# Performance work log

Measured on AMD Instinct MI355X. Metric: run time of the kernel, lower is better.

Reference implementation:

```python
import jax, jax.numpy as jnp
import numpy as np

B, S, HID = 2, 2048, 1024
H, D = 16, 64
KD = H * D
RMS_EPS = 1e-5
L2_EPS = 1e-12


def setup_inputs() -> dict:
    key = jax.random.key(0)
    ks = jax.random.split(key, 9)
    w = lambda k, shape: jax.random.normal(k, shape, jnp.float32) * 0.02
    return {
        "x": jax.random.normal(ks[0], (B, S, HID), jnp.float32),
        "Wq": w(ks[1], (HID, KD)),
        "Wk": w(ks[2], (HID, KD)),
        "Wv": w(ks[3], (HID, KD)),
        "Wf": w(ks[4], (HID, KD)),
        "Wb": w(ks[5], (HID, H)),
        "A_log": jnp.log(jnp.full((H,), 8.0, jnp.float32)),
        "dt_bias": jnp.zeros((KD,), jnp.float32),
        "Wg": w(ks[6], (HID, KD)),
        "bg": jnp.zeros((KD,), jnp.float32),
        "Wo": w(ks[7], (KD, HID)),
        "norm_w": jnp.ones((D,), jnp.float32),
    }


def _l2norm(t):
    n = jnp.sqrt(jnp.sum(t * t, axis=-1, keepdims=True))
    return t / jnp.clip(n, L2_EPS)


def reference(x, Wq, Wk, Wv, Wf, Wb, A_log, dt_bias, Wg, bg, Wo, norm_w):
    b, s, _ = x.shape
    h = A_log.shape[0]
    d = norm_w.shape[0]

    q = jax.nn.silu(x @ Wq).reshape(b, s, h, d)
    k = jax.nn.silu(x @ Wk).reshape(b, s, h, d)
    v = jax.nn.silu(x @ Wv).reshape(b, s, h, d)
    g = (x @ Wf).reshape(b, s, h, d)
    beta = jax.nn.sigmoid(x @ Wb)  # [b,s,h]

    q = _l2norm(q)
    k = _l2norm(k)
    g = jax.nn.sigmoid(g - dt_bias.reshape(h, d))
    A = jnp.exp(-jnp.exp(A_log))  # [h]

    # seq-major for scan: [s, b, h, d]
    qs = jnp.moveaxis(q, 1, 0)
    kss = jnp.moveaxis(k, 1, 0)
    vs = jnp.moveaxis(v, 1, 0)
    gs = jnp.moveaxis(g, 1, 0)
    bs = jnp.moveaxis(beta, 1, 0)  # [s,b,h]

    state0 = jnp.zeros((b, h, d, d), x.dtype)

    def step(state, inp):
        q_t, k_t, v_t, g_t, b_t = inp
        o_t = jnp.einsum('bhd,bhde->bhe', q_t, state) * g_t
        state = A[None, :, None, None] * state \
            + b_t[..., None, None] * (k_t[..., :, None] * v_t[..., None, :])
        return state, o_t

    _, o = jax.lax.scan(step, state0, (qs, kss, vs, gs, bs))
    o = jnp.moveaxis(o, 0, 1)  # [b,s,h,d]

    # RMSNorm over head_dim, then gate
    o = o * jax.lax.rsqrt(jnp.mean(o * o, axis=-1, keepdims=True) + RMS_EPS) * norm_w
    gate = jax.nn.sigmoid(x @ Wg + bg).reshape(b, s, h, d)
    o = (o * gate).reshape(b, s, h * d)
    return o @ Wo
```

## Files before the change

kernel.cpp:

```cpp
#include <hip/hip_runtime.h>
#include <hip/hip_bf16.h>

typedef __hip_bfloat16 bf16;
typedef __attribute__((ext_vector_type(8))) short v8s;
typedef __attribute__((ext_vector_type(4))) short v4s;
typedef __attribute__((ext_vector_type(4))) float v4f;

#define MFMA16(a,b,c) __builtin_amdgcn_mfma_f32_16x16x32_bf16((a),(b),(c),0,0,0)
#define SCHED0() __builtin_amdgcn_sched_barrier(0)


static const size_t OFF_XBF    = 0;
static const size_t OFF_WCATT  = 8388608;
static const size_t OFF_WOT    = OFF_WCATT + 11010048;
static const size_t OFF_Y      = OFF_WOT + 2097152;
static const size_t OFF_BETA   = OFF_Y + 41943040;
static const size_t OFF_OPRE   = OFF_XBF;

__device__ __forceinline__ void gl2lds16(const bf16* g, bf16* l) {
  __builtin_amdgcn_global_load_lds(
      (const __attribute__((address_space(1))) void*)g,
      (__attribute__((address_space(3))) void*)l, 16, 0, 0);
}

__global__ __launch_bounds__(256) void prep(
    const float* __restrict__ x,
    const float* __restrict__ W0, const float* __restrict__ W1,
    const float* __restrict__ W2, const float* __restrict__ W3,
    const float* __restrict__ W4, const float* __restrict__ W5,
    const float* __restrict__ Wb,
    bf16* __restrict__ xb, bf16* __restrict__ WcatT, bf16* __restrict__ WoT)
{
  __shared__ float tile[64][65];
  int bid = blockIdx.x;
  if (bid < 2048) {
    int t = bid * 256 + threadIdx.x;
    int row = t >> 7, ch = t & 127;
    const float* src = x + (size_t)row * 1024 + ch * 8;
    v4f v0 = *(const v4f*)src;
    v4f v1 = *(const v4f*)(src + 4);
    union { bf16 h[8]; v8s s; } u;
    for (int i = 0; i < 4; ++i) { u.h[i] = __float2bfloat16(v0[i]); u.h[4+i] = __float2bfloat16(v1[i]); }
    int ch2 = (ch & ~3) | ((ch ^ (row >> 1)) & 3);
    *(v8s*)(xb + (size_t)row * 1024 + ch2 * 8) = u.s;
  } else if (bid < 3584) {
    int b2 = bid - 2048;
    int mi = b2 >> 8;
    int rem = b2 & 255;
    int c0 = (rem & 15) * 64;
    int r0 = (rem >> 4) * 64;
    const float* W = (mi==0)?W0:(mi==1)?W1:(mi==2)?W2:(mi==3)?W3:(mi==4)?W4:W5;
    bf16* out = (mi < 5) ? (WcatT + (size_t)mi * 1048576) : WoT;
    int l = threadIdx.x & 63, w = threadIdx.x >> 6;
    for (int i = 0; i < 16; ++i)
      tile[w + 4*i][l] = W[(size_t)(r0 + w + 4*i) * 1024 + c0 + l];
    __syncthreads();
    for (int i = 0; i < 16; ++i) {
      int orow = c0 + w + 4*i;
      int q = l >> 3;
      int q2 = (mi < 5) ? ((q & ~3) | ((q ^ (orow >> 1)) & 3))
                        : ((q ^ orow) & 7);
      int col = r0 + (q2 << 3) + (l & 7);
      out[(size_t)orow * 1024 + col] = __float2bfloat16(tile[l][w + 4*i]);
    }
  } else {
    int j = (bid - 3584) * 2 + (threadIdx.x >> 7);
    int ch = threadIdx.x & 127;
    union { bf16 h[8]; v8s s; } u;
    for (int i = 0; i < 8; ++i)
      u.h[i] = __float2bfloat16(j < 16 ? Wb[(size_t)(ch*8 + i) * 16 + j] : 0.f);
    int row = 5120 + j;
    int ch2 = (ch & ~3) | ((ch ^ (row >> 1)) & 3);
    *(v8s*)(WcatT + (size_t)row * 1024 + ch2 * 8) = u.s;
  }
}

__global__ __launch_bounds__(256, 2) void gemm_main(
    const bf16* __restrict__ A, const bf16* __restrict__ BT,
    bf16* __restrict__ Yb, const float* __restrict__ dtb,
    const float* __restrict__ bgp, float* __restrict__ betaOut)
{
  __shared__ bf16 As[2][4096];
  __shared__ bf16 Bs[2][8192];
  const int tid = threadIdx.x;
  const int xcd = (int)blockIdx.x & 7, p = (int)blockIdx.x >> 3;
  const int by = xcd * 4 + (p & 3);
  const int bx = p >> 2;
  const int m0 = by * 128, n0 = bx * 256;
  const int w = tid >> 6, l = tid & 63;
  const int wr = w >> 1, wc = w & 1;
  const int lr = l & 15, lkq = l >> 4;
  const int cq = ((lkq ^ ((lr >> 1) & 3)) << 3);
  const int arow0 = (wr * 64 + lr) * 32;
  const int brow0 = (wc * 128 + lr) * 32;

  v4f acc[4][8];
  #pragma unroll
  for (int i = 0; i < 4; ++i)
    #pragma unroll
    for (int j = 0; j < 8; ++j) acc[i][j] = (v4f){0.f,0.f,0.f,0.f};

#define STG(t_, buf_) do { \
  gl2lds16(&A[(size_t)(m0 + (tid >> 2)) * 1024 + (t_)*32 + (tid & 3)*8], \
           &As[buf_][tid*8]); \
  gl2lds16(&A[(size_t)(m0 + 64 + (tid >> 2)) * 1024 + (t_)*32 + (tid & 3)*8], \
           &As[buf_][2048 + tid*8]); \
  gl2lds16(&BT[(size_t)(n0 + (tid >> 2)) * 1024 + (t_)*32 + (tid & 3)*8], \
           &Bs[buf_][tid*8]); \
  gl2lds16(&BT[(size_t)(n0 + 64 + (tid >> 2)) * 1024 + (t_)*32 + (tid & 3)*8], \
           &Bs[buf_][2048 + tid*8]); \
  gl2lds16(&BT[(size_t)(n0 + 128 + (tid >> 2)) * 1024 + (t_)*32 + (tid & 3)*8], \
           &Bs[buf_][4096 + tid*8]); \
  gl2lds16(&BT[(size_t)(n0 + 192 + (tid >> 2)) * 1024 + (t_)*32 + (tid & 3)*8], \
           &Bs[buf_][6144 + tid*8]); \
} while(0)

  STG(0, 0); SCHED0();
  STG(1, 1); SCHED0();

  for (int t = 0; t < 32; ++t) {
    const int cur = t & 1;
    if (t == 31) { asm volatile("s_waitcnt vmcnt(0)" ::: "memory"); }
    else         { asm volatile("s_waitcnt vmcnt(6)" ::: "memory"); }
    SCHED0();
    __builtin_amdgcn_s_barrier();
    SCHED0();
    const bf16* Ab = &As[cur][0];
    const bf16* Bb = &Bs[cur][0];
    v8s afr[4], bfr[8];
    #pragma unroll
    for (int mt = 0; mt < 4; ++mt)
      afr[mt] = *(const v8s*)(Ab + arow0 + mt*512 + cq);
    #pragma unroll
    for (int nt = 0; nt < 8; ++nt)
      bfr[nt] = *(const v8s*)(Bb + brow0 + nt*512 + cq);
    asm volatile("s_waitcnt lgkmcnt(0)" ::: "memory");
    SCHED0();
    __builtin_amdgcn_s_barrier();
    SCHED0();
    if (t + 2 < 32) { STG(t + 2, cur); }
    __builtin_amdgcn_s_setprio(1);
    #pragma unroll
    for (int mt = 0; mt < 4; ++mt)
      #pragma unroll
      for (int nt = 0; nt < 8; ++nt)
        acc[mt][nt] = MFMA16(afr[mt], bfr[nt], acc[mt][nt]);
    __builtin_amdgcn_s_setprio(0);
  }
#undef STG

  const int region = (n0 + wc * 128) >> 10;
  #pragma unroll
  for (int mt = 0; mt < 4; ++mt)
    #pragma unroll
    for (int r = 0; r < 4; ++r) {
      int gm = m0 + wr * 64 + mt * 16 + lkq * 4 + r;
      float v[8];
      if (region < 2) {
        #pragma unroll
        for (int hh = 0; hh < 2; ++hh) {
          float ss = 0.f;
          #pragma unroll
          for (int q4 = 0; q4 < 4; ++q4) {
            float y = acc[mt][hh*4 + q4][r];
            float s = y / (1.f + __expf(-y));
            v[hh*4 + q4] = s; ss += s * s;
          }
          ss += __shfl_xor(ss, 1, 64); ss += __shfl_xor(ss, 2, 64);
          ss += __shfl_xor(ss, 4, 64); ss += __shfl_xor(ss, 8, 64);
          float inv = 1.f / fmaxf(sqrtf(ss), 1e-12f);
          #pragma unroll
          for (int q4 = 0; q4 < 4; ++q4) v[hh*4 + q4] *= inv;
        }
      } else if (region == 2) {
        #pragma unroll
        for (int nt = 0; nt < 8; ++nt) {
          float y = acc[mt][nt][r];
          v[nt] = y / (1.f + __expf(-y));
        }
      } else if (region == 3) {
        #pragma unroll
        for (int nt = 0; nt < 8; ++nt) {
          int gn = n0 + wc * 128 + nt * 16 + lr;
          float z = acc[mt][nt][r] - dtb[gn & 1023];
          v[nt] = 1.f / (1.f + __expf(-z));
        }
      } else if (region == 4) {
        #pragma unroll
        for (int nt = 0; nt < 8; ++nt) {
          int gn = n0 + wc * 128 + nt * 16 + lr;
          float z = acc[mt][nt][r] + bgp[gn & 1023];
          v[nt] = 1.f / (1.f + __expf(-z));
        }
      } else {
        #pragma unroll
        for (int nt = 0; nt < 8; ++nt) {
          int gn = n0 + wc * 128 + nt * 16 + lr;
          if (gn < 5136)
            betaOut[(size_t)gm * 16 + (gn - 5120)] =
                1.f / (1.f + __expf(-acc[mt][nt][r]));
        }
        continue;
      }
      #pragma unroll
      for (int nt = 0; nt < 8; ++nt) {
        int gn = n0 + wc * 128 + nt * 16 + lr;
        Yb[(size_t)gm * 5120 + gn] = __float2bfloat16(v[nt]);
      }
    }
}

__global__ __launch_bounds__(256) void gemm_out(
    const bf16* __restrict__ A, const bf16* __restrict__ BT,
    float* __restrict__ Co)
{
  __shared__ bf16 As[2][8192];
  __shared__ bf16 Bs[2][8192];
  const int tid = threadIdx.x;
  int swzb = ((int)blockIdx.x & 7) * 32 + ((int)blockIdx.x >> 3);
  const int by = swzb >> 3, bx = swzb & 7;
  const int m0 = by * 128, n0 = bx * 128;
  const int w = tid >> 6, l = tid & 63;
  const int wm = (w >> 1) * 64, wn = (w & 1) * 64;
  const int lr = l & 15, lkq = l >> 4;
  const int xorv = lr & 7;
  const int c0 = ((lkq ^ xorv) << 3), c1 = (((4 + lkq) ^ xorv) << 3);
  v4f acc[4][4];
  for (int i = 0; i < 4; ++i) for (int j = 0; j < 4; ++j) acc[i][j] = (v4f){0.f,0.f,0.f,0.f};

#define STAGE(kk, buf) \
  for (int i_ = 0; i_ < 4; ++i_) { \
    int eo_ = (i_ * 256 + tid) * 8; \
    int r_ = eo_ >> 6, cc_ = eo_ & 63; \
    gl2lds16(&A[(size_t)(m0 + r_) * 1024 + (kk) + cc_], &As[buf][eo_]); \
    gl2lds16(&BT[(size_t)(n0 + r_) * 1024 + (kk) + cc_], &Bs[buf][eo_]); \
  }

  STAGE(0, 0);
  __syncthreads();
  int cur = 0;
  for (int kk = 0; kk < 1024; kk += 64) {
    if (kk + 64 < 1024) { STAGE(kk + 64, cur ^ 1); }
    v8s af[2][4], bfr[2][4];
    #pragma unroll
    for (int mt = 0; mt < 4; ++mt) {
      af[0][mt] = *(const v8s*)(&As[cur][(wm + mt*16 + lr) * 64 + c0]);
      af[1][mt] = *(const v8s*)(&As[cur][(wm + mt*16 + lr) * 64 + c1]);
      bfr[0][mt] = *(const v8s*)(&Bs[cur][(wn + mt*16 + lr) * 64 + c0]);
      bfr[1][mt] = *(const v8s*)(&Bs[cur][(wn + mt*16 + lr) * 64 + c1]);
    }
    #pragma unroll
    for (int kc = 0; kc < 2; ++kc)
      #pragma unroll
      for (int mt = 0; mt < 4; ++mt)
        #pragma unroll
        for (int nt = 0; nt < 4; ++nt)
          acc[mt][nt] = MFMA16(af[kc][mt], bfr[kc][nt], acc[mt][nt]);
    __syncthreads();
    cur ^= 1;
  }
#undef STAGE
  #pragma unroll
  for (int mt = 0; mt < 4; ++mt)
    #pragma unroll
    for (int nt = 0; nt < 4; ++nt)
      #pragma unroll
      for (int r = 0; r < 4; ++r) {
        int gm = m0 + wm + mt*16 + lkq*4 + r;
        int gn = n0 + wn + nt*16 + lr;
        Co[(size_t)gm * 1024 + gn] = acc[mt][nt][r];
      }
}

__global__ __launch_bounds__(256) void passFused(
    const bf16* __restrict__ Y, const float* __restrict__ beta,
    const float* __restrict__ A_log, const float* __restrict__ norm_w,
    bf16* __restrict__ opre)
{
  int c = blockIdx.x, bh = blockIdx.y;
  int b = bh >> 4, h = bh & 15;
  int row0 = b * 2048 + c * 64;
  int prow0 = row0 - 64;
  bool hasPrev = (c > 0);
  __shared__ bf16 Qs[64][72], Ks[64][72], Vt[64][72];
  __shared__ bf16 Kp[64][72], Vp[64][72];
  __shared__ bf16 Ps[64][72], St[64][72];
  __shared__ float betas[64], pw[64];
  int tid = threadIdx.x, w = tid >> 6, l = tid & 63;
  float aexp = __expf(A_log[h]);
  if (tid < 64) {
    pw[tid] = __expf(-aexp * (float)tid);
    betas[tid] = beta[(size_t)(row0 + tid) * 16 + h];
  }
  __syncthreads();
  for (int i = 0; i < 2; ++i) {
    int cid = i * 256 + tid;
    int r = cid >> 3, c8 = (cid & 7) * 8;
    size_t ybase = (size_t)(row0 + r) * 5120 + h * 64 + c8;
    v8s q8 = *(const v8s*)(&Y[ybase]);
    v8s k8 = *(const v8s*)(&Y[ybase + 1024]);
    v8s v8 = *(const v8s*)(&Y[ybase + 2048]);
    *(v8s*)(&Qs[r][c8]) = q8;
    *(v8s*)(&Ks[r][c8]) = k8;
    const bf16* vpt = (const bf16*)&v8;
    for (int jj = 0; jj < 8; ++jj) Vt[c8 + jj][r] = vpt[jj];
    if (hasPrev) {
      size_t pbase = (size_t)(prow0 + r) * 5120 + h * 64 + c8;
      v8s pk8 = *(const v8s*)(&Y[pbase + 1024]);
      v8s pv8 = *(const v8s*)(&Y[pbase + 2048]);
      float coefT = pw[63 - r] * beta[(size_t)(prow0 + r) * 16 + h];
      const bf16* pkp = (const bf16*)&pk8;
      const bf16* pvp = (const bf16*)&pv8;
      for (int jj = 0; jj < 8; ++jj) {
        Kp[c8 + jj][r] = __float2bfloat16(coefT * __bfloat162float(pkp[jj]));
        Vp[c8 + jj][r] = pvp[jj];
      }
    } else {
      bf16 z = __float2bfloat16(0.f);
      for (int jj = 0; jj < 8; ++jj) { Kp[c8 + jj][r] = z; Vp[c8 + jj][r] = z; }
    }
  }
  __syncthreads();
  const int lr = l & 15, lk = (l >> 4) * 8;
  v4f accT[4], accP[4];
  for (int nt = 0; nt < 4; ++nt) { accT[nt] = (v4f){0.f,0.f,0.f,0.f}; accP[nt] = (v4f){0.f,0.f,0.f,0.f}; }
  for (int kc = 0; kc < 2; ++kc) {
    v8s av = *(const v8s*)(&Vp[w*16 + lr][kc*32 + lk]);
    v8s aq = *(const v8s*)(&Qs[w*16 + lr][kc*32 + lk]);
    for (int nt = 0; nt < 4; ++nt) {
      v8s bk = *(const v8s*)(&Kp[nt*16 + lr][kc*32 + lk]);
      v8s bc = *(const v8s*)(&Ks[nt*16 + lr][kc*32 + lk]);
      accT[nt] = MFMA16(av, bk, accT[nt]);
      accP[nt] = MFMA16(aq, bc, accP[nt]);
    }
  }
  for (int nt = 0; nt < 4; ++nt)
    for (int r = 0; r < 4; ++r) {
      int row = w*16 + (l>>4)*4 + r;
      int col = nt*16 + lr;
      St[row][col] = __float2bfloat16(accT[nt][r]);
      float v = accP[nt][r];
      float pm = (col < row) ? v * betas[col] * pw[row - 1 - col] : 0.f;
      Ps[row][col] = __float2bfloat16(pm);
    }
  __syncthreads();
  v4f accO[4], accI[4];
  for (int nt = 0; nt < 4; ++nt) { accO[nt] = (v4f){0.f,0.f,0.f,0.f}; accI[nt] = (v4f){0.f,0.f,0.f,0.f}; }
  for (int kc = 0; kc < 2; ++kc) {
    v8s ap = *(const v8s*)(&Ps[w*16 + lr][kc*32 + lk]);
    v8s aq = *(const v8s*)(&Qs[w*16 + lr][kc*32 + lk]);
    for (int nt = 0; nt < 4; ++nt) {
      v8s bv = *(const v8s*)(&Vt[nt*16 + lr][kc*32 + lk]);
      v8s bs = *(const v8s*)(&St[nt*16 + lr][kc*32 + lk]);
      accO[nt] = MFMA16(ap, bv, accO[nt]);
      accI[nt] = MFMA16(aq, bs, accI[nt]);
    }
  }
  for (int r = 0; r < 4; ++r) {
    int tq = w*16 + (l>>4)*4 + r;
    float sc = pw[tq];
    size_t orow = (size_t)(row0 + tq);
    float o[4];
    float ss = 0.f;
    for (int nt = 0; nt < 4; ++nt) {
      int e = nt*16 + lr;
      float v = accO[nt][r] + sc * accI[nt][r];
      float g = __bfloat162float(Y[orow * 5120 + 3072 + h*64 + e]);
      v *= g;
      o[nt] = v;
      ss += v * v;
    }
    ss += __shfl_xor(ss, 1, 64);
    ss += __shfl_xor(ss, 2, 64);
    ss += __shfl_xor(ss, 4, 64);
    ss += __shfl_xor(ss, 8, 64);
    float rms = rsqrtf(ss * (1.f/64.f) + 1e-5f);
    for (int nt = 0; nt < 4; ++nt) {
      int e = nt*16 + lr;
      float gate = __bfloat162float(Y[orow * 5120 + 4096 + h*64 + e]);
      float outv = o[nt] * rms * norm_w[e] * gate;
      int col = h*64 + ((((e >> 3)) ^ ((int)orow & 7)) << 3) + (e & 7);
      opre[orow * 1024 + col] = __float2bfloat16(outv);
    }
  }
}

extern "C" void kernel_launch(void* const* d_in, const int* in_sizes, int n_in,
                              void* d_out, int out_size, void* d_ws, size_t ws_size,
                              hipStream_t stream) {
  const float* x       = (const float*)d_in[0];
  const float* Wq      = (const float*)d_in[1];
  const float* Wk      = (const float*)d_in[2];
  const float* Wv      = (const float*)d_in[3];
  const float* Wf      = (const float*)d_in[4];
  const float* Wb      = (const float*)d_in[5];
  const float* A_log   = (const float*)d_in[6];
  const float* dt_bias = (const float*)d_in[7];
  const float* Wg      = (const float*)d_in[8];
  const float* bg      = (const float*)d_in[9];
  const float* Wo      = (const float*)d_in[10];
  const float* norm_w  = (const float*)d_in[11];

  char* ws = (char*)d_ws;
  bf16*  xb     = (bf16*)(ws + OFF_XBF);
  bf16*  wcatT  = (bf16*)(ws + OFF_WCATT);
  bf16*  woT    = (bf16*)(ws + OFF_WOT);
  bf16*  Y      = (bf16*)(ws + OFF_Y);
  float* beta   = (float*)(ws + OFF_BETA);
  bf16*  opre   = (bf16*)(ws + OFF_OPRE);

  prep<<<3712, 256, 0, stream>>>(x, Wq, Wk, Wv, Wf, Wg, Wo, Wb, xb, wcatT, woT);
  gemm_main<<<672, 256, 0, stream>>>(xb, wcatT, Y, dt_bias, bg, beta);
  passFused<<<dim3(32, 32), 256, 0, stream>>>(Y, beta, A_log, norm_w, opre);
  gemm_out<<<256, 256, 0, stream>>>(opre, woT, (float*)d_out);
}
```

Before: 131.8 us.

## Retile output GEMM to 64x128 with K32 stages and gemm_main swizzle layout

Rewrites gemm_out to use 64x128 tiles with 32-wide K steps, doubling the grid to 512 blocks. It uses an explicit vmcnt-based double-buffer pipeline with split barriers and MFMA priority boosting. The WoT and opre layouts switch to the same 4-chunk XOR swizzle used by gemm_main so the new LDS reads avoid bank conflicts. The aim is to fill more CUs and overlap loads with compute, at the cost of less data reuse per block and more barriers per K step.

```diff
diff --git a/kernel.cpp b/kernel.cpp
--- a/kernel.cpp
+++ b/kernel.cpp
@@ -57,10 +57,9 @@
     __syncthreads();
     for (int i = 0; i < 16; ++i) {
       int orow = c0 + w + 4*i;
-      int q = l >> 3;
-      int q2 = (mi < 5) ? ((q & ~3) | ((q ^ (orow >> 1)) & 3))
-                        : ((q ^ orow) & 7);
-      int col = r0 + (q2 << 3) + (l & 7);
+      int q = (r0 >> 3) + (l >> 3);
+      int q2 = (q & ~3) | ((q ^ (orow >> 1)) & 3);
+      int col = (q2 << 3) + (l & 7);
       out[(size_t)orow * 1024 + col] = __float2bfloat16(tile[l][w + 4*i]);
     }
   } else {
@@ -214,60 +213,76 @@
     const bf16* __restrict__ A, const bf16* __restrict__ BT,
     float* __restrict__ Co)
 {
-  __shared__ bf16 As[2][8192];
-  __shared__ bf16 Bs[2][8192];
+  __shared__ bf16 As[2][2048];
+  __shared__ bf16 Bs[2][4096];
   const int tid = threadIdx.x;
-  int swzb = ((int)blockIdx.x & 7) * 32 + ((int)blockIdx.x >> 3);
-  const int by = swzb >> 3, bx = swzb & 7;
-  const int m0 = by * 128, n0 = bx * 128;
+  const int by = (int)blockIdx.x >> 3;
+  const int bx = (int)blockIdx.x & 7;
+  const int m0 = by * 64, n0 = bx * 128;
   const int w = tid >> 6, l = tid & 63;
-  const int wm = (w >> 1) * 64, wn = (w & 1) * 64;
+  const int wr = w >> 1, wc = w & 1;
   const int lr = l & 15, lkq = l >> 4;
-  const int xorv = lr & 7;
-  const int c0 = ((lkq ^ xorv) << 3), c1 = (((4 + lkq) ^ xorv) << 3);
-  v4f acc[4][4];
-  for (int i = 0; i < 4; ++i) for (int j = 0; j < 4; ++j) acc[i][j] = (v4f){0.f,0.f,0.f,0.f};
-
-#define STAGE(kk, buf) \
-  for (int i_ = 0; i_ < 4; ++i_) { \
-    int eo_ = (i_ * 256 + tid) * 8; \
-    int r_ = eo_ >> 6, cc_ = eo_ & 63; \
-    gl2lds16(&A[(size_t)(m0 + r_) * 1024 + (kk) + cc_], &As[buf][eo_]); \
-    gl2lds16(&BT[(size_t)(n0 + r_) * 1024 + (kk) + cc_], &Bs[buf][eo_]); \
-  }
-
-  STAGE(0, 0);
-  __syncthreads();
-  int cur = 0;
-  for (int kk = 0; kk < 1024; kk += 64) {
-    if (kk + 64 < 1024) { STAGE(kk + 64, cur ^ 1); }
-    v8s af[2][4], bfr[2][4];
-    #pragma unroll
-    for (int mt = 0; mt < 4; ++mt) {
-      af[0][mt] = *(const v8s*)(&As[cur][(wm + mt*16 + lr) * 64 + c0]);
-      af[1][mt] = *(const v8s*)(&As[cur][(wm + mt*16 + lr) * 64 + c1]);
-      bfr[0][mt] = *(const v8s*)(&Bs[cur][(wn + mt*16 + lr) * 64 + c0]);
-      bfr[1][mt] = *(const v8s*)(&Bs[cur][(wn + mt*16 + lr) * 64 + c1]);
-    }
-    #pragma unroll
-    for (int kc = 0; kc < 2; ++kc)
+  const int cq = ((lkq ^ ((lr >> 1) & 3)) << 3);
+  const int arow0 = (wr * 32 + lr) * 32;
+  const int brow0 = (wc * 64 + lr) * 32;
+
+  v4f acc[2][4];
+  #pragma unroll
+  for (int i = 0; i < 2; ++i)
+    #pragma unroll
+    for (int j = 0; j < 4; ++j) acc[i][j] = (v4f){0.f,0.f,0.f,0.f};
+
+#define STG(t_, buf_) do { \
+  gl2lds16(&A[(size_t)(m0 + (tid >> 2)) * 1024 + (t_)*32 + (tid & 3)*8], \
+           &As[buf_][tid*8]); \
+  gl2lds16(&BT[(size_t)(n0 + (tid >> 2)) * 1024 + (t_)*32 + (tid & 3)*8], \
+           &Bs[buf_][tid*8]); \
+  gl2lds16(&BT[(size_t)(n0 + 64 + (tid >> 2)) * 1024 + (t_)*32 + (tid & 3)*8], \
+           &Bs[buf_][2048 + tid*8]); \
+} while(0)
+
+  STG(0, 0); SCHED0();
+  STG(1, 1); SCHED0();
+
+  for (int t = 0; t < 32; ++t) {
+    const int cur = t & 1;
+    if (t == 31) { asm volatile("s_waitcnt vmcnt(0)" ::: "memory"); }
+    else         { asm volatile("s_waitcnt vmcnt(3)" ::: "memory"); }
+    SCHED0();
+    __builtin_amdgcn_s_barrier();
+    SCHED0();
+    const bf16* Ab = &As[cur][0];
+    const bf16* Bb = &Bs[cur][0];
+    v8s afr[2], bfr[4];
+    #pragma unroll
+    for (int mt = 0; mt < 2; ++mt)
+      afr[mt] = *(const v8s*)(Ab + arow0 + mt*512 + cq);
+    #pragma unroll
+    for (int nt = 0; nt < 4; ++nt)
+      bfr[nt] = *(const v8s*)(Bb + brow0 + nt*512 + cq);
+    asm volatile("s_waitcnt lgkmcnt(0)" ::: "memory");
+    SCHED0();
+    __builtin_amdgcn_s_barrier();
+    SCHED0();
+    if (t + 2 < 32) { STG(t + 2, cur); }
+    __builtin_amdgcn_s_setprio(1);
+    #pragma unroll
+    for (int mt = 0; mt < 2; ++mt)
       #pragma unroll
-      for (int mt = 0; mt < 4; ++mt)
-        #pragma unroll
-        for (int nt = 0; nt < 4; ++nt)
-          acc[mt][nt] = MFMA16(af[kc][mt], bfr[kc][nt], acc[mt][nt]);
-    __syncthreads();
-    cur ^= 1;
-  }
-#undef STAGE
+      for (int nt = 0; nt < 4; ++nt)
+        acc[mt][nt] = MFMA16(afr[mt], bfr[nt], acc[mt][nt]);
+    __builtin_amdgcn_s_setprio(0);
+  }
+#undef STG
+
   #pragma unroll
-  for (int mt = 0; mt < 4; ++mt)
+  for (int mt = 0; mt < 2; ++mt)
     #pragma unroll
     for (int nt = 0; nt < 4; ++nt)
       #pragma unroll
       for (int r = 0; r < 4; ++r) {
-        int gm = m0 + wm + mt*16 + lkq*4 + r;
-        int gn = n0 + wn + nt*16 + lr;
+        int gm = m0 + wr * 32 + mt * 16 + lkq * 4 + r;
+        int gn = n0 + wc * 64 + nt * 16 + lr;
         Co[(size_t)gm * 1024 + gn] = acc[mt][nt][r];
       }
 }
@@ -379,8 +394,9 @@
       int e = nt*16 + lr;
       float gate = __bfloat162float(Y[orow * 5120 + 4096 + h*64 + e]);
       float outv = o[nt] * rms * norm_w[e] * gate;
-      int col = h*64 + ((((e >> 3)) ^ ((int)orow & 7)) << 3) + (e & 7);
-      opre[orow * 1024 + col] = __float2bfloat16(outv);
+      int ch = h*8 + (e >> 3);
+      int ch2 = (ch & ~3) | ((ch ^ ((int)orow >> 1)) & 3);
+      opre[orow * 1024 + ch2*8 + (e & 7)] = __float2bfloat16(outv);
     }
   }
 }
@@ -412,5 +428,5 @@
   prep<<<3712, 256, 0, stream>>>(x, Wq, Wk, Wv, Wf, Wg, Wo, Wb, xb, wcatT, woT);
   gemm_main<<<672, 256, 0, stream>>>(xb, wcatT, Y, dt_bias, bg, beta);
   passFused<<<dim3(32, 32), 256, 0, stream>>>(Y, beta, A_log, norm_w, opre);
-  gemm_out<<<256, 256, 0, stream>>>(opre, woT, (float*)d_out);
-}
+  gemm_out<<<512, 256, 0, stream>>>(opre, woT, (float*)d_out);
+}
```

Result: no change. 129.3 us (median of 2 runs) (-1.9%).
